# Kernel tuning notes

Measured on AMD Instinct MI355X. Metric: run time of the kernel, lower is better.

Reference implementation:

```python
import jax, jax.numpy as jnp
import numpy as np

N, E, G, H, L, GD = 100000, 1600000, 64, 128, 3, 32
NEG_SLOPE = 0.2
EPS = 1e-5


def setup_inputs() -> dict:
    key = jax.random.key(0)
    ks = jax.random.split(key, 10)
    s = 1.0 / np.sqrt(H)
    return {
        "x": jax.random.normal(ks[0], (N, H), jnp.float32),
        "global_feat": jax.random.normal(ks[1], (G, GD), jnp.float32),
        "W_src": jax.random.normal(ks[2], (L, H, H), jnp.float32) * s,
        "W_dst": jax.random.normal(ks[3], (L, H, H), jnp.float32) * s,
        "att": jax.random.normal(ks[4], (L, H), jnp.float32) * s,
        "b_conv": jnp.zeros((L, H), jnp.float32),
        "gn_w": jnp.ones((L, H), jnp.float32),
        "gn_b": jnp.zeros((L, H), jnp.float32),
        "gn_ms": jnp.ones((L, H), jnp.float32),
        "W1": jax.random.normal(ks[5], (H * L + GD, H), jnp.float32) * (1.0 / np.sqrt(H * L + GD)),
        "b1": jnp.zeros((H,), jnp.float32),
        "W2": jax.random.normal(ks[6], (H, 1), jnp.float32) * s,
        "b2": jnp.zeros((1,), jnp.float32),
        "edge_index": jax.random.randint(ks[7], (2, E), 0, N, jnp.int64),
        "batch": jnp.sort(jax.random.randint(ks[8], (N,), 0, G, jnp.int64)),
    }


def reference(x, global_feat, W_src, W_dst, att, b_conv, gn_w, gn_b, gn_ms,
              W1, b1, W2, b2, edge_index, batch):
    n = x.shape[0]
    g = global_feat.shape[0]
    layers = W_src.shape[0]
    loops = jnp.arange(n, dtype=edge_index.dtype)
    src = jnp.concatenate([edge_index[0], loops])  # add_self_loops=True
    dst = jnp.concatenate([edge_index[1], loops])
    counts = jnp.maximum(
        jax.ops.segment_sum(jnp.ones((n,), x.dtype), batch, num_segments=g), 1.0)

    outs = []
    for l in range(layers):
        # --- GATv2Conv (heads=1) ---
        xl = x @ W_src[l]          # source transform [N,H]
        xr = x @ W_dst[l]          # target transform [N,H]
        e = jax.nn.leaky_relu(xl[src] + xr[dst], NEG_SLOPE) @ att[l]  # [Etot]
        emax = jax.ops.segment_max(e, dst, num_segments=n)
        ex = jnp.exp(e - emax[dst])
        denom = jax.ops.segment_sum(ex, dst, num_segments=n)
        alpha = ex / denom[dst]
        h = jax.ops.segment_sum(alpha[:, None] * xl[src], dst, num_segments=n) + b_conv[l]
        # --- GraphNorm ---
        mean = jax.ops.segment_sum(h, batch, num_segments=g) / counts[:, None]
        sub = h - gn_ms[l] * mean[batch]
        var = jax.ops.segment_sum(sub * sub, batch, num_segments=g) / counts[:, None]
        h = gn_w[l] * sub * jax.lax.rsqrt(var[batch] + EPS) + gn_b[l]
        x = jax.nn.relu(h)
        # --- global_mean_pool ---
        outs.append(jax.ops.segment_sum(x, batch, num_segments=g) / counts[:, None])

    hcat = jnp.concatenate(outs + [global_feat], axis=1)  # JK cat + global feats
    z = jax.nn.relu(hcat @ W1 + b1)  # dropout = identity (eval)
    return z @ W2 + b2
```

## Files before the change

### kernel.cpp

```cpp
#include <hip/hip_runtime.h>
#include <hip/hip_bf16.h>
#include <math.h>

#define N_    100000
#define E_    1600000
#define ETOT_ 1700000
#define G_    64
#define H_    128
#define L_    3
#define GD_   32
#define NEG_  0.2f
#define EPS_  1e-5f

#define NBUK_ 391
#define CH_   8192
#define MCH_  196

typedef unsigned short ushort_t;
typedef unsigned int uint_t;
typedef __attribute__((ext_vector_type(4))) float f32x4;
typedef __attribute__((ext_vector_type(8))) short bf16x8;
typedef __attribute__((ext_vector_type(8))) unsigned short ushort8;

__device__ __forceinline__ ushort_t bfb(float f) {
    __hip_bfloat16 h = __float2bfloat16(f);
    return *reinterpret_cast<ushort_t*>(&h);
}


__global__ void k_init(float* pooled, int* gstart, const int* __restrict__ batch) {
    int i = blockIdx.x * 256 + threadIdx.x;
    if (i < L_ * G_ * H_) pooled[i] = 0.f;
    if (i <= G_) {
        int lo = 0, hi = N_;
        while (lo < hi) { int mid = (lo + hi) >> 1; if (batch[mid] < i) lo = mid + 1; else hi = mid; }
        gstart[i] = lo;
    }
}


__global__ __launch_bounds__(256) void k_bcount(const int* __restrict__ edst, int* __restrict__ C) {
    __shared__ int hist[NBUK_];
    int t = threadIdx.x, m = blockIdx.x;
    for (int i = t; i < NBUK_; i += 256) hist[i] = 0;
    __syncthreads();
    int base = m * CH_;
#pragma unroll
    for (int j = 0; j < CH_ / 256; j++) {
        int e = base + j * 256 + t;
        if (e < E_) atomicAdd(&hist[edst[e] >> 8], 1);
    }
    __syncthreads();
    for (int i = t; i < NBUK_; i += 256) C[i * MCH_ + m] = hist[i];
}

__global__ __launch_bounds__(256) void k_bscan(int* __restrict__ C, int* __restrict__ bucketEdges) {
    __shared__ int arr[256];
    int b = blockIdx.x, t = threadIdx.x;
    int v = (t < MCH_) ? C[b * MCH_ + t] : 0;
    arr[t] = v;
    __syncthreads();
    for (int off = 1; off < 256; off <<= 1) {
        int x = (t >= off) ? arr[t - off] : 0;
        __syncthreads();
        arr[t] += x;
        __syncthreads();
    }
    if (t < MCH_) C[b * MCH_ + t] = arr[t] - v;
    if (t == 255) bucketEdges[b] = arr[255];
}

__global__ __launch_bounds__(512) void k_bscan2(const int* __restrict__ bucketEdges,
                                                int* __restrict__ bstartE, int* __restrict__ bstartT,
                                                int* __restrict__ rowptr) {
    __shared__ int aE[512], aT[512];
    int t = threadIdx.x;
    int e = 0, tot = 0;
    if (t < NBUK_) {
        e = bucketEdges[t];
        int nib = N_ - t * 256; if (nib > 256) nib = 256;
        tot = e + nib;
    }
    aE[t] = e; aT[t] = tot;
    __syncthreads();
    for (int off = 1; off < 512; off <<= 1) {
        int xe = (t >= off) ? aE[t - off] : 0;
        int xt = (t >= off) ? aT[t - off] : 0;
        __syncthreads();
        aE[t] += xe; aT[t] += xt;
        __syncthreads();
    }
    if (t < NBUK_) { bstartE[t] = aE[t] - e; bstartT[t] = aT[t] - tot; }
    if (t == 0) rowptr[N_] = ETOT_;
}

__global__ __launch_bounds__(256) void k_bscatter(const int* __restrict__ esrc, const int* __restrict__ edst,
                                                  const int* __restrict__ C, const int* __restrict__ bstartE,
                                                  int2* __restrict__ stag) {
    __shared__ int cur[NBUK_];
    int t = threadIdx.x, m = blockIdx.x;
    for (int i = t; i < NBUK_; i += 256) cur[i] = C[i * MCH_ + m] + bstartE[i];
    __syncthreads();
    int base = m * CH_;
#pragma unroll
    for (int j = 0; j < CH_ / 256; j++) {
        int e = base + j * 256 + t;
        if (e < E_) {
            int s = esrc[e], d = edst[e];
            int pos = atomicAdd(&cur[d >> 8], 1);
            int2 p; p.x = s; p.y = d;
            stag[pos] = p;
        }
    }
}

__global__ __launch_bounds__(256) void k_bfinal(const int2* __restrict__ stag,
                                                const int* __restrict__ bucketEdges,
                                                const int* __restrict__ bstartE, const int* __restrict__ bstartT,
                                                int* __restrict__ rowptr, int* __restrict__ colarr) {
    __shared__ int deg[256];
    __shared__ int cursor[256];
    int b = blockIdx.x, t = threadIdx.x;
    int nb0 = b * 256;
    int nib = N_ - nb0; if (nib > 256) nib = 256;
    int ebeg = bstartE[b], ecnt = bucketEdges[b];
    deg[t] = (t < nib) ? 1 : 0;
    __syncthreads();
    for (int i = t; i < ecnt; i += 256) {
        int2 p = stag[ebeg + i];
        atomicAdd(&deg[p.y - nb0], 1);
    }
    __syncthreads();
    int v = deg[t];
    cursor[t] = v;
    __syncthreads();
    for (int off = 1; off < 256; off <<= 1) {
        int x = (t >= off) ? cursor[t - off] : 0;
        __syncthreads();
        cursor[t] += x;
        __syncthreads();
    }
    int excl = cursor[t] - v;
    int rowbase = bstartT[b];
    if (t < nib) {
        rowptr[nb0 + t] = rowbase + excl;
        colarr[rowbase + excl] = nb0 + t;
    }
    __syncthreads();
    cursor[t] = excl + 1;
    __syncthreads();
    for (int i = t; i < ecnt; i += 256) {
        int2 p = stag[ebeg + i];
        int pos = atomicAdd(&cursor[p.y - nb0], 1);
        colarr[rowbase + pos] = p.x;
    }
}


__global__ void k_cvt(const float* __restrict__ x, ushort_t* __restrict__ xb) {
    int i = blockIdx.x * 256 + threadIdx.x;
    float4 v = *(const float4*)(x + (size_t)i * 4);
    ushort4 o;
    o.x = bfb(v.x); o.y = bfb(v.y); o.z = bfb(v.z); o.w = bfb(v.w);
    *(ushort4*)(xb + (size_t)i * 4) = o;
}

__global__ void k_prep_w(const float* __restrict__ Ws, const float* __restrict__ Wd,
                         ushort_t* __restrict__ Wt) {
    int i = blockIdx.x * 256 + threadIdx.x;
    if (i >= L_ * 256 * H_) return;
    int l = i >> 15;
    int r = i & 32767;
    int c = r >> 7, k = r & 127;
    float v = (c < H_) ? Ws[(size_t)l * H_ * H_ + k * H_ + c]
                       : Wd[(size_t)l * H_ * H_ + k * H_ + (c - H_)];
    Wt[i] = bfb(v);
}


__global__ __launch_bounds__(256) void k_mfma(const ushort_t* __restrict__ xb,
                                              const ushort_t* __restrict__ Wt,
                                              ushort_t* __restrict__ xlb,
                                              float* __restrict__ xr) {
    int wv = threadIdx.x >> 6, lane = threadIdx.x & 63;
    int wt = blockIdx.x * 4 + wv;
    int row0 = wt * 16;
    if (row0 >= N_) return;
    int sl = lane & 15, q = lane >> 4;

    bf16x8 a[4];
    const ushort_t* ap = xb + (size_t)(row0 + sl) * H_ + q * 8;
#pragma unroll
    for (int kk = 0; kk < 4; kk++) a[kk] = *(const bf16x8*)(ap + kk * 32);

    f32x4 acc[16];
#pragma unroll
    for (int c = 0; c < 16; c++) acc[c] = (f32x4){0.f, 0.f, 0.f, 0.f};

#pragma unroll
    for (int c = 0; c < 16; c++) {
        const ushort_t* bp = Wt + (size_t)(c * 16 + sl) * H_ + q * 8;
#pragma unroll
        for (int kk = 0; kk < 4; kk++) {
            bf16x8 b = *(const bf16x8*)(bp + kk * 32);
            acc[c] = __builtin_amdgcn_mfma_f32_16x16x32_bf16(a[kk], b, acc[c], 0, 0, 0);
        }
    }

    int orow = row0 + q * 4;
#pragma unroll
    for (int c = 0; c < 8; c++)
#pragma unroll
        for (int j = 0; j < 4; j++)
            xlb[(size_t)(orow + j) * H_ + c * 16 + sl] = bfb(acc[c][j]);
#pragma unroll
    for (int c = 8; c < 16; c++)
#pragma unroll
        for (int j = 0; j < 4; j++)
            xr[(size_t)(orow + j) * H_ + (c - 8) * 16 + sl] = acc[c][j];
}


__global__ __launch_bounds__(256) void k_conv(const ushort_t* __restrict__ xlb, const float* __restrict__ xr,
                                              const int* __restrict__ rowptr, const int* __restrict__ colarr,
                                              const float* __restrict__ attl, const float* __restrict__ bcl,
                                              float* __restrict__ h) {
    int tid = threadIdx.x;
    int lane = tid & 63, wv = tid >> 6;
    int sl = lane & 15, q = lane >> 4;
    int row = blockIdx.x * 16 + wv * 4 + q;
    int d0 = sl * 8;

    float xrv[8], av[8], av5[8];
    {
        float4 t0 = *(const float4*)(xr + (size_t)row * H_ + d0);
        float4 t1 = *(const float4*)(xr + (size_t)row * H_ + d0 + 4);
        xrv[0] = t0.x; xrv[1] = t0.y; xrv[2] = t0.z; xrv[3] = t0.w;
        xrv[4] = t1.x; xrv[5] = t1.y; xrv[6] = t1.z; xrv[7] = t1.w;
        float4 a0 = *(const float4*)(attl + d0);
        float4 a1 = *(const float4*)(attl + d0 + 4);
        av[0] = a0.x; av[1] = a0.y; av[2] = a0.z; av[3] = a0.w;
        av[4] = a1.x; av[5] = a1.y; av[6] = a1.z; av[7] = a1.w;
#pragma unroll
        for (int e = 0; e < 8; e++) av5[e] = NEG_ * av[e];
    }

    int jb = rowptr[row];
    int n = rowptr[row + 1] - jb;

    float ssum = 0.f;
    float ac[8] = {0.f, 0.f, 0.f, 0.f, 0.f, 0.f, 0.f, 0.f};

    int s = (n > 0) ? colarr[jb] : 0;
    for (int i = 0; i < n; i++) {
        int snext = (i + 1 < n) ? colarr[jb + i + 1] : 0;
        ushort8 u = *(const ushort8*)(xlb + (size_t)s * H_ + d0);
        float v[8];
        float p = 0.f;
#pragma unroll
        for (int e = 0; e < 8; e++) {
            v[e] = __uint_as_float(((uint_t)u[e]) << 16);
            float t = v[e] + xrv[e];
            p = fmaf(t, (t > 0.f ? av[e] : av5[e]), p);
        }
        p += __shfl_xor(p, 8);
        p += __shfl_xor(p, 4);
        p += __shfl_xor(p, 2);
        p += __shfl_xor(p, 1);
        float wgt = __expf(p);
        ssum += wgt;
#pragma unroll
        for (int e = 0; e < 8; e++) ac[e] = fmaf(wgt, v[e], ac[e]);
        s = snext;
    }

    float inv = 1.f / ssum;
    float4 b0 = *(const float4*)(bcl + d0);
    float4 b1 = *(const float4*)(bcl + d0 + 4);
    float4 o0 = { ac[0] * inv + b0.x, ac[1] * inv + b0.y, ac[2] * inv + b0.z, ac[3] * inv + b0.w };
    float4 o1 = { ac[4] * inv + b1.x, ac[5] * inv + b1.y, ac[6] * inv + b1.z, ac[7] * inv + b1.w };
    *(float4*)(h + (size_t)row * H_ + d0) = o0;
    *(float4*)(h + (size_t)row * H_ + d0 + 4) = o1;
}


__global__ void k_zero_gn(float* gsum, float* gsq) {
    int i = blockIdx.x * 256 + threadIdx.x;
    if (i < G_ * H_) { gsum[i] = 0.f; gsq[i] = 0.f; }
}

__global__ void k_gn_stat(const float* __restrict__ h, const int* __restrict__ batch,
                          float* gsum, float* gsq) {
    int tid = threadIdx.x;
    int nb = blockIdx.x * 64;
    int d = tid & 127, hh = tid >> 7;
    int nend = nb + 64; if (nend > N_) nend = N_;
    float s1 = 0.f, s2 = 0.f; int curg = -1;
    for (int n = nb + hh; n < nend; n += 2) {
        int g = batch[n];
        if (g != curg) {
            if (curg >= 0) { atomicAdd(&gsum[curg * H_ + d], s1); atomicAdd(&gsq[curg * H_ + d], s2); }
            s1 = 0.f; s2 = 0.f; curg = g;
        }
        float v = h[(size_t)n * H_ + d];
        s1 += v; s2 += v * v;
    }
    if (curg >= 0) { atomicAdd(&gsum[curg * H_ + d], s1); atomicAdd(&gsq[curg * H_ + d], s2); }
}

__global__ void k_gn_fin(float* gsum, float* gsq, const int* __restrict__ gstart,
                         const float* __restrict__ gnwl, const float* __restrict__ gnmsl) {
    int i = blockIdx.x * 256 + threadIdx.x;
    if (i < G_ * H_) {
        int g = i >> 7, d = i & 127;
        int c = gstart[g + 1] - gstart[g]; if (c < 1) c = 1;
        float ic = 1.f / (float)c;
        float mean = gsum[i] * ic;
        float e2   = gsq[i] * ic;
        float ms = gnmsl[d];
        float var = e2 - ms * (2.f - ms) * mean * mean;
        gsum[i] = ms * mean;
        gsq[i]  = gnwl[d] * rsqrtf(var + EPS_);
    }
}

__global__ void k_gn_apply(const float* __restrict__ h, const int* __restrict__ batch,
                           const float* __restrict__ gmv, const float* __restrict__ giv,
                           const float* __restrict__ gnbl,
                           ushort_t* __restrict__ hb, float* pooled_l) {
    int tid = threadIdx.x;
    int nb = blockIdx.x * 64;
    int d = tid & 127, hh = tid >> 7;
    int nend = nb + 64; if (nend > N_) nend = N_;
    float bb = gnbl[d];
    float pacc = 0.f; int curg = -1; float mv = 0.f, iv = 0.f;
    for (int n = nb + hh; n < nend; n += 2) {
        int g = batch[n];
        if (g != curg) {
            if (curg >= 0) atomicAdd(&pooled_l[curg * H_ + d], pacc);
            pacc = 0.f; curg = g;
            mv = gmv[g * H_ + d];
            iv = giv[g * H_ + d];
        }
        float v = (h[(size_t)n * H_ + d] - mv) * iv + bb;
        v = fmaxf(v, 0.f);
        hb[(size_t)n * H_ + d] = bfb(v);
        pacc += v;
    }
    if (curg >= 0) atomicAdd(&pooled_l[curg * H_ + d], pacc);
}


__global__ __launch_bounds__(128) void k_mlp(const float* __restrict__ pooled, const float* __restrict__ gfeat,
                                             const int* __restrict__ gstart,
                                             const float* __restrict__ W1, const float* __restrict__ b1,
                                             const float* __restrict__ W2, const float* __restrict__ b2,
                                             float* __restrict__ out) {
    int g = blockIdx.x;
    int c = threadIdx.x;
    __shared__ float hc[H_ * L_ + GD_];
    __shared__ float zz[H_];
    int cn = gstart[g + 1] - gstart[g]; if (cn < 1) cn = 1;
    float ic = 1.f / (float)cn;
    for (int k = c; k < H_ * L_; k += 128)
        hc[k] = pooled[(k >> 7) * G_ * H_ + g * H_ + (k & 127)] * ic;
    if (c < GD_) hc[H_ * L_ + c] = gfeat[g * GD_ + c];
    __syncthreads();
    float z = b1[c];
#pragma unroll 4
    for (int k = 0; k < H_ * L_ + GD_; k++)
        z += hc[k] * W1[k * H_ + c];
    z = fmaxf(z, 0.f);
    zz[c] = z * W2[c];
    __syncthreads();
    for (int off = 64; off > 0; off >>= 1) {
        if (c < off) zz[c] += zz[c + off];
        __syncthreads();
    }
    if (c == 0) out[g] = zz[0] + b2[0];
}


extern "C" void kernel_launch(void* const* d_in, const int* in_sizes, int n_in,
                              void* d_out, int out_size, void* d_ws, size_t ws_size,
                              hipStream_t stream) {
    const float* x0    = (const float*)d_in[0];
    const float* gfeat = (const float*)d_in[1];
    const float* Wsrc  = (const float*)d_in[2];
    const float* Wdst  = (const float*)d_in[3];
    const float* att   = (const float*)d_in[4];
    const float* bconv = (const float*)d_in[5];
    const float* gnw   = (const float*)d_in[6];
    const float* gnb   = (const float*)d_in[7];
    const float* gnms  = (const float*)d_in[8];
    const float* W1    = (const float*)d_in[9];
    const float* b1    = (const float*)d_in[10];
    const float* W2    = (const float*)d_in[11];
    const float* b2    = (const float*)d_in[12];
    const int*   eidx  = (const int*)d_in[13];
    const int*   batch = (const int*)d_in[14];
    const int* esrc = eidx;
    const int* edst = eidx + E_;
    float* out = (float*)d_out;

    char* w = (char*)d_ws;
    size_t off = 0;
    auto alloc = [&](size_t bytes) { char* p = w + off; off += (bytes + 255) & ~(size_t)255; return p; };
    ushort_t* xb    = (ushort_t*)alloc((size_t)N_ * H_ * 2);
    ushort_t* xlb   = (ushort_t*)alloc((size_t)N_ * H_ * 2);
    float* xr     = (float*)alloc((size_t)N_ * H_ * 4);
    float* hbuf   = (float*)alloc((size_t)N_ * H_ * 4);
    ushort_t* Wt    = (ushort_t*)alloc((size_t)L_ * 256 * H_ * 2);
    int*   rowptr = (int*)alloc((size_t)(N_ + 1) * 4);
    int*   colarr = (int*)alloc((size_t)ETOT_ * 4);
    int*   bktE   = (int*)alloc(NBUK_ * 4);
    int*   bstartE= (int*)alloc(NBUK_ * 4);
    int*   bstartT= (int*)alloc(NBUK_ * 4);
    int*   gstart = (int*)alloc((G_ + 1) * 4);
    float* gsum   = (float*)alloc(G_ * H_ * 4);
    float* gsq    = (float*)alloc(G_ * H_ * 4);
    float* pooled = (float*)alloc((size_t)L_ * G_ * H_ * 4);
    int2* stag = (int2*)xr;
    int*  C    = (int*)hbuf;
    (void)ws_size; (void)in_sizes; (void)n_in; (void)out_size;

    k_init<<<(N_ + 255) / 256, 256, 0, stream>>>(pooled, gstart, batch);
    k_bcount<<<MCH_, 256, 0, stream>>>(edst, C);
    k_bscan<<<NBUK_, 256, 0, stream>>>(C, bktE);
    k_bscan2<<<1, 512, 0, stream>>>(bktE, bstartE, bstartT, rowptr);
    k_bscatter<<<MCH_, 256, 0, stream>>>(esrc, edst, C, bstartE, stag);
    k_bfinal<<<NBUK_, 256, 0, stream>>>(stag, bktE, bstartE, bstartT, rowptr, colarr);

    k_cvt<<<(N_ * H_ / 4 + 255) / 256, 256, 0, stream>>>(x0, xb);
    k_prep_w<<<(L_ * 256 * H_ + 255) / 256, 256, 0, stream>>>(Wsrc, Wdst, Wt);

    for (int l = 0; l < L_; l++) {
        k_mfma<<<(N_ / 16 + 3) / 4, 256, 0, stream>>>(xb, Wt + (size_t)l * 256 * H_, xlb, xr);
        k_conv<<<N_ / 16, 256, 0, stream>>>(xlb, xr, rowptr, colarr,
                                            att + (size_t)l * H_, bconv + (size_t)l * H_, hbuf);
        k_zero_gn<<<(G_ * H_ + 255) / 256, 256, 0, stream>>>(gsum, gsq);
        k_gn_stat<<<(N_ + 63) / 64, 256, 0, stream>>>(hbuf, batch, gsum, gsq);
        k_gn_fin<<<(G_ * H_ + 255) / 256, 256, 0, stream>>>(gsum, gsq, gstart,
                                                            gnw + (size_t)l * H_, gnms + (size_t)l * H_);
        k_gn_apply<<<(N_ + 63) / 64, 256, 0, stream>>>(hbuf, batch, gsum, gsq,
                                                       gnb + (size_t)l * H_, xb,
                                                       pooled + (size_t)l * G_ * H_);
    }

    k_mlp<<<G_, 128, 0, stream>>>(pooled, gfeat, gstart, W1, b1, W2, b2, out);
}
```

Baseline: 645.1 us.

## Fuse GraphNorm stats into conv, apply norm in next GEMM, store bf16 intermediates

Folds the GraphNorm statistic accumulation into the attention conv epilogue, using block-level shared reductions when all 16 rows share a graph. The normalize+ReLU step moves into the next layer's MFMA input load, so the pooling kernel only reads h and no longer writes xb. The x-to-bf16 conversion is folded into the first GEMM. xr and h are now stored as bf16 instead of fp32, which lowers memory traffic at some precision cost. The edge-bucketing chunk size is also shrunk to give more blocks. The aim is fewer kernel launches and fewer full passes over N×H arrays, at the cost of statistics computed from fp32 values while h is stored rounded to bf16.

```diff
diff --git a/kernel.cpp b/kernel.cpp
--- a/kernel.cpp
+++ b/kernel.cpp
@@ -7,14 +7,15 @@
 #define ETOT_ 1700000
 #define G_    64
 #define H_    128
+#define GH_   8192
 #define L_    3
 #define GD_   32
 #define NEG_  0.2f
 #define EPS_  1e-5f
 
 #define NBUK_ 391
-#define CH_   8192
-#define MCH_  196
+#define CH_   2048
+#define MCH_  782
 
 typedef unsigned short ushort_t;
 typedef unsigned int uint_t;
@@ -26,11 +27,15 @@
     __hip_bfloat16 h = __float2bfloat16(f);
     return *reinterpret_cast<ushort_t*>(&h);
 }
-
-
-__global__ void k_init(float* pooled, int* gstart, const int* __restrict__ batch) {
+__device__ __forceinline__ float uf(ushort_t u) {
+    return __uint_as_float(((uint_t)u) << 16);
+}
+
+
+__global__ void k_init(float* pooled, float* gsum, float* gsq, int* gstart,
+                       const int* __restrict__ batch) {
     int i = blockIdx.x * 256 + threadIdx.x;
-    if (i < L_ * G_ * H_) pooled[i] = 0.f;
+    if (i < L_ * GH_) { pooled[i] = 0.f; gsum[i] = 0.f; gsq[i] = 0.f; }
     if (i <= G_) {
         int lo = 0, hi = N_;
         while (lo < hi) { int mid = (lo + hi) >> 1; if (batch[mid] < i) lo = mid + 1; else hi = mid; }
@@ -54,20 +59,20 @@
     for (int i = t; i < NBUK_; i += 256) C[i * MCH_ + m] = hist[i];
 }
 
-__global__ __launch_bounds__(256) void k_bscan(int* __restrict__ C, int* __restrict__ bucketEdges) {
-    __shared__ int arr[256];
+__global__ __launch_bounds__(1024) void k_bscan(int* __restrict__ C, int* __restrict__ bucketEdges) {
+    __shared__ int arr[1024];
     int b = blockIdx.x, t = threadIdx.x;
     int v = (t < MCH_) ? C[b * MCH_ + t] : 0;
     arr[t] = v;
     __syncthreads();
-    for (int off = 1; off < 256; off <<= 1) {
+    for (int off = 1; off < 1024; off <<= 1) {
         int x = (t >= off) ? arr[t - off] : 0;
         __syncthreads();
         arr[t] += x;
         __syncthreads();
     }
     if (t < MCH_) C[b * MCH_ + t] = arr[t] - v;
-    if (t == 255) bucketEdges[b] = arr[255];
+    if (t == 1023) bucketEdges[b] = arr[1023];
 }
 
 __global__ __launch_bounds__(512) void k_bscan2(const int* __restrict__ bucketEdges,
@@ -157,14 +162,6 @@
 }
 
 
-__global__ void k_cvt(const float* __restrict__ x, ushort_t* __restrict__ xb) {
-    int i = blockIdx.x * 256 + threadIdx.x;
-    float4 v = *(const float4*)(x + (size_t)i * 4);
-    ushort4 o;
-    o.x = bfb(v.x); o.y = bfb(v.y); o.z = bfb(v.z); o.w = bfb(v.w);
-    *(ushort4*)(xb + (size_t)i * 4) = o;
-}
-
 __global__ void k_prep_w(const float* __restrict__ Ws, const float* __restrict__ Wd,
                          ushort_t* __restrict__ Wt) {
     int i = blockIdx.x * 256 + threadIdx.x;
@@ -178,20 +175,63 @@
 }
 
 
-__global__ __launch_bounds__(256) void k_mfma(const ushort_t* __restrict__ xb,
-                                              const ushort_t* __restrict__ Wt,
-                                              ushort_t* __restrict__ xlb,
-                                              float* __restrict__ xr) {
+template<int FIRST>
+__global__ __launch_bounds__(256) void k_mfma_t(const float* __restrict__ x0,
+                                                const ushort_t* __restrict__ hin,
+                                                const int* __restrict__ batch,
+                                                const float* __restrict__ mv,
+                                                const float* __restrict__ iv,
+                                                const float* __restrict__ bb,
+                                                const ushort_t* __restrict__ Wt,
+                                                ushort_t* __restrict__ xlb,
+                                                ushort_t* __restrict__ xrb) {
     int wv = threadIdx.x >> 6, lane = threadIdx.x & 63;
-    int wt = blockIdx.x * 4 + wv;
-    int row0 = wt * 16;
+    int row0 = (blockIdx.x * 4 + wv) * 16;
     if (row0 >= N_) return;
     int sl = lane & 15, q = lane >> 4;
+    int row = row0 + sl;
 
     bf16x8 a[4];
-    const ushort_t* ap = xb + (size_t)(row0 + sl) * H_ + q * 8;
-#pragma unroll
-    for (int kk = 0; kk < 4; kk++) a[kk] = *(const bf16x8*)(ap + kk * 32);
+    if (FIRST) {
+        const float* ap = x0 + (size_t)row * H_ + q * 8;
+#pragma unroll
+        for (int kk = 0; kk < 4; kk++) {
+            float4 v0 = *(const float4*)(ap + kk * 32);
+            float4 v1 = *(const float4*)(ap + kk * 32 + 4);
+            bf16x8 t;
+            t[0] = (short)bfb(v0.x); t[1] = (short)bfb(v0.y);
+            t[2] = (short)bfb(v0.z); t[3] = (short)bfb(v0.w);
+            t[4] = (short)bfb(v1.x); t[5] = (short)bfb(v1.y);
+            t[6] = (short)bfb(v1.z); t[7] = (short)bfb(v1.w);
+            a[kk] = t;
+        }
+    } else {
+        int g = batch[row];
+        const ushort_t* hp = hin + (size_t)row * H_ + q * 8;
+        const float* mvp = mv + g * H_ + q * 8;
+        const float* ivp = iv + g * H_ + q * 8;
+        const float* bbp = bb + q * 8;
+#pragma unroll
+        for (int kk = 0; kk < 4; kk++) {
+            ushort8 u = *(const ushort8*)(hp + kk * 32);
+            float4 m0 = *(const float4*)(mvp + kk * 32);
+            float4 m1 = *(const float4*)(mvp + kk * 32 + 4);
+            float4 i0 = *(const float4*)(ivp + kk * 32);
+            float4 i1 = *(const float4*)(ivp + kk * 32 + 4);
+            float4 c0 = *(const float4*)(bbp + kk * 32);
+            float4 c1 = *(const float4*)(bbp + kk * 32 + 4);
+            bf16x8 t;
+            t[0] = (short)bfb(fmaxf((uf(u[0]) - m0.x) * i0.x + c0.x, 0.f));
+            t[1] = (short)bfb(fmaxf((uf(u[1]) - m0.y) * i0.y + c0.y, 0.f));
+            t[2] = (short)bfb(fmaxf((uf(u[2]) - m0.z) * i0.z + c0.z, 0.f));
+            t[3] = (short)bfb(fmaxf((uf(u[3]) - m0.w) * i0.w + c0.w, 0.f));
+            t[4] = (short)bfb(fmaxf((uf(u[4]) - m1.x) * i1.x + c1.x, 0.f));
+            t[5] = (short)bfb(fmaxf((uf(u[5]) - m1.y) * i1.y + c1.y, 0.f));
+            t[6] = (short)bfb(fmaxf((uf(u[6]) - m1.z) * i1.z + c1.z, 0.f));
+            t[7] = (short)bfb(fmaxf((uf(u[7]) - m1.w) * i1.w + c1.w, 0.f));
+            a[kk] = t;
+        }
+    }
 
     f32x4 acc[16];
 #pragma unroll
@@ -217,15 +257,22 @@
     for (int c = 8; c < 16; c++)
 #pragma unroll
         for (int j = 0; j < 4; j++)
-            xr[(size_t)(orow + j) * H_ + (c - 8) * 16 + sl] = acc[c][j];
-}
-
-
-__global__ __launch_bounds__(256) void k_conv(const ushort_t* __restrict__ xlb, const float* __restrict__ xr,
+            xrb[(size_t)(orow + j) * H_ + (c - 8) * 16 + sl] = bfb(acc[c][j]);
+}
+
+
+__global__ __launch_bounds__(256) void k_conv(const ushort_t* __restrict__ xlb,
+                                              const ushort_t* __restrict__ xrb,
                                               const int* __restrict__ rowptr, const int* __restrict__ colarr,
                                               const float* __restrict__ attl, const float* __restrict__ bcl,
-                                              float* __restrict__ h) {
+                                              const int* __restrict__ batch,
+                                              ushort_t* __restrict__ h,
+                                              float* __restrict__ gsum, float* __restrict__ gsq) {
+    __shared__ float ls1[H_], ls2[H_];
     int tid = threadIdx.x;
+    if (tid < H_) { ls1[tid] = 0.f; ls2[tid] = 0.f; }
+    __syncthreads();
+
     int lane = tid & 63, wv = tid >> 6;
     int sl = lane & 15, q = lane >> 4;
     int row = blockIdx.x * 16 + wv * 4 + q;
@@ -233,16 +280,13 @@
 
     float xrv[8], av[8], av5[8];
     {
-        float4 t0 = *(const float4*)(xr + (size_t)row * H_ + d0);
-        float4 t1 = *(const float4*)(xr + (size_t)row * H_ + d0 + 4);
-        xrv[0] = t0.x; xrv[1] = t0.y; xrv[2] = t0.z; xrv[3] = t0.w;
-        xrv[4] = t1.x; xrv[5] = t1.y; xrv[6] = t1.z; xrv[7] = t1.w;
+        ushort8 ux = *(const ushort8*)(xrb + (size_t)row * H_ + d0);
         float4 a0 = *(const float4*)(attl + d0);
         float4 a1 = *(const float4*)(attl + d0 + 4);
         av[0] = a0.x; av[1] = a0.y; av[2] = a0.z; av[3] = a0.w;
         av[4] = a1.x; av[5] = a1.y; av[6] = a1.z; av[7] = a1.w;
 #pragma unroll
-        for (int e = 0; e < 8; e++) av5[e] = NEG_ * av[e];
+        for (int e = 0; e < 8; e++) { xrv[e] = uf(ux[e]); av5[e] = NEG_ * av[e]; }
     }
 
     int jb = rowptr[row];
@@ -259,7 +303,7 @@
         float p = 0.f;
 #pragma unroll
         for (int e = 0; e < 8; e++) {
-            v[e] = __uint_as_float(((uint_t)u[e]) << 16);
+            v[e] = uf(u[e]);
             float t = v[e] + xrv[e];
             p = fmaf(t, (t > 0.f ? av[e] : av5[e]), p);
         }
@@ -277,41 +321,54 @@
     float inv = 1.f / ssum;
     float4 b0 = *(const float4*)(bcl + d0);
     float4 b1 = *(const float4*)(bcl + d0 + 4);
-    float4 o0 = { ac[0] * inv + b0.x, ac[1] * inv + b0.y, ac[2] * inv + b0.z, ac[3] * inv + b0.w };
-    float4 o1 = { ac[4] * inv + b1.x, ac[5] * inv + b1.y, ac[6] * inv + b1.z, ac[7] * inv + b1.w };
-    *(float4*)(h + (size_t)row * H_ + d0) = o0;
-    *(float4*)(h + (size_t)row * H_ + d0 + 4) = o1;
-}
-
-
-__global__ void k_zero_gn(float* gsum, float* gsq) {
-    int i = blockIdx.x * 256 + threadIdx.x;
-    if (i < G_ * H_) { gsum[i] = 0.f; gsq[i] = 0.f; }
-}
-
-__global__ void k_gn_stat(const float* __restrict__ h, const int* __restrict__ batch,
-                          float* gsum, float* gsq) {
-    int tid = threadIdx.x;
-    int nb = blockIdx.x * 64;
-    int d = tid & 127, hh = tid >> 7;
-    int nend = nb + 64; if (nend > N_) nend = N_;
-    float s1 = 0.f, s2 = 0.f; int curg = -1;
-    for (int n = nb + hh; n < nend; n += 2) {
-        int g = batch[n];
-        if (g != curg) {
-            if (curg >= 0) { atomicAdd(&gsum[curg * H_ + d], s1); atomicAdd(&gsq[curg * H_ + d], s2); }
-            s1 = 0.f; s2 = 0.f; curg = g;
-        }
-        float v = h[(size_t)n * H_ + d];
-        s1 += v; s2 += v * v;
-    }
-    if (curg >= 0) { atomicAdd(&gsum[curg * H_ + d], s1); atomicAdd(&gsq[curg * H_ + d], s2); }
-}
+    float o[8];
+    o[0] = ac[0] * inv + b0.x; o[1] = ac[1] * inv + b0.y;
+    o[2] = ac[2] * inv + b0.z; o[3] = ac[3] * inv + b0.w;
+    o[4] = ac[4] * inv + b1.x; o[5] = ac[5] * inv + b1.y;
+    o[6] = ac[6] * inv + b1.z; o[7] = ac[7] * inv + b1.w;
+
+    ushort8 ho;
+#pragma unroll
+    for (int e = 0; e < 8; e++) ho[e] = bfb(o[e]);
+    *(ushort8*)(h + (size_t)row * H_ + d0) = ho;
+
+    float s1[8], s2[8];
+#pragma unroll
+    for (int e = 0; e < 8; e++) { s1[e] = o[e]; s2[e] = o[e] * o[e]; }
+
+    int g0 = batch[blockIdx.x * 16];
+    int g1 = batch[blockIdx.x * 16 + 15];
+    if (g0 == g1) {
+#pragma unroll
+        for (int e = 0; e < 8; e++) {
+            s1[e] += __shfl_xor(s1[e], 16); s1[e] += __shfl_xor(s1[e], 32);
+            s2[e] += __shfl_xor(s2[e], 16); s2[e] += __shfl_xor(s2[e], 32);
+        }
+        if (q == 0) {
+#pragma unroll
+            for (int e = 0; e < 8; e++) {
+                atomicAdd(&ls1[d0 + e], s1[e]);
+                atomicAdd(&ls2[d0 + e], s2[e]);
+            }
+        }
+        __syncthreads();
+        if (tid < H_) atomicAdd(&gsum[g0 * H_ + tid], ls1[tid]);
+        else if (tid < 2 * H_) atomicAdd(&gsq[g0 * H_ + tid - H_], ls2[tid - H_]);
+    } else {
+        int g = batch[row];
+#pragma unroll
+        for (int e = 0; e < 8; e++) {
+            atomicAdd(&gsum[g * H_ + d0 + e], s1[e]);
+            atomicAdd(&gsq[g * H_ + d0 + e], s2[e]);
+        }
+    }
+}
+
 
 __global__ void k_gn_fin(float* gsum, float* gsq, const int* __restrict__ gstart,
                          const float* __restrict__ gnwl, const float* __restrict__ gnmsl) {
     int i = blockIdx.x * 256 + threadIdx.x;
-    if (i < G_ * H_) {
+    if (i < GH_) {
         int g = i >> 7, d = i & 127;
         int c = gstart[g + 1] - gstart[g]; if (c < 1) c = 1;
         float ic = 1.f / (float)c;
@@ -324,30 +381,39 @@
     }
 }
 
-__global__ void k_gn_apply(const float* __restrict__ h, const int* __restrict__ batch,
-                           const float* __restrict__ gmv, const float* __restrict__ giv,
-                           const float* __restrict__ gnbl,
-                           ushort_t* __restrict__ hb, float* pooled_l) {
+
+__global__ void k_pool(const ushort_t* __restrict__ h, const int* __restrict__ batch,
+                       const float* __restrict__ mv, const float* __restrict__ iv,
+                       const float* __restrict__ bb, float* __restrict__ pooled_l) {
     int tid = threadIdx.x;
     int nb = blockIdx.x * 64;
-    int d = tid & 127, hh = tid >> 7;
+    int d2 = (tid & 63) * 2, hh = tid >> 6;
     int nend = nb + 64; if (nend > N_) nend = N_;
-    float bb = gnbl[d];
-    float pacc = 0.f; int curg = -1; float mv = 0.f, iv = 0.f;
-    for (int n = nb + hh; n < nend; n += 2) {
+    float b0 = bb[d2], b1 = bb[d2 + 1];
+    float p0 = 0.f, p1 = 0.f; int curg = -1;
+    float m0 = 0.f, m1 = 0.f, i0 = 0.f, i1 = 0.f;
+    for (int n = nb + hh; n < nend; n += 4) {
         int g = batch[n];
         if (g != curg) {
-            if (curg >= 0) atomicAdd(&pooled_l[curg * H_ + d], pacc);
-            pacc = 0.f; curg = g;
-            mv = gmv[g * H_ + d];
-            iv = giv[g * H_ + d];
-        }
-        float v = (h[(size_t)n * H_ + d] - mv) * iv + bb;
-        v = fmaxf(v, 0.f);
-        hb[(size_t)n * H_ + d] = bfb(v);
-        pacc += v;
-    }
-    if (curg >= 0) atomicAdd(&pooled_l[curg * H_ + d], pacc);
+            if (curg >= 0) {
+                atomicAdd(&pooled_l[curg * H_ + d2], p0);
+                atomicAdd(&pooled_l[curg * H_ + d2 + 1], p1);
+            }
+            p0 = 0.f; p1 = 0.f; curg = g;
+            m0 = mv[g * H_ + d2]; m1 = mv[g * H_ + d2 + 1];
+            i0 = iv[g * H_ + d2]; i1 = iv[g * H_ + d2 + 1];
+        }
+        uint_t u = *(const uint_t*)(h + (size_t)n * H_ + d2);
+        float v0 = __uint_as_float(u << 16);
+        float v1 = __uint_as_float(u & 0xffff0000u);
+        v0 = fmaxf((v0 - m0) * i0 + b0, 0.f);
+        v1 = fmaxf((v1 - m1) * i1 + b1, 0.f);
+        p0 += v0; p1 += v1;
+    }
+    if (curg >= 0) {
+        atomicAdd(&pooled_l[curg * H_ + d2], p0);
+        atomicAdd(&pooled_l[curg * H_ + d2 + 1], p1);
+    }
 }
 
 
@@ -363,7 +429,7 @@
     int cn = gstart[g + 1] - gstart[g]; if (cn < 1) cn = 1;
     float ic = 1.f / (float)cn;
     for (int k = c; k < H_ * L_; k += 128)
-        hc[k] = pooled[(k >> 7) * G_ * H_ + g * H_ + (k & 127)] * ic;
+        hc[k] = pooled[(k >> 7) * GH_ + g * H_ + (k & 127)] * ic;
     if (c < GD_) hc[H_ * L_ + c] = gfeat[g * GD_ + c];
     __syncthreads();
     float z = b1[c];
@@ -406,45 +472,51 @@
     char* w = (char*)d_ws;
     size_t off = 0;
     auto alloc = [&](size_t bytes) { char* p = w + off; off += (bytes + 255) & ~(size_t)255; return p; };
-    ushort_t* xb    = (ushort_t*)alloc((size_t)N_ * H_ * 2);
-    ushort_t* xlb   = (ushort_t*)alloc((size_t)N_ * H_ * 2);
-    float* xr     = (float*)alloc((size_t)N_ * H_ * 4);
-    float* hbuf   = (float*)alloc((size_t)N_ * H_ * 4);
-    ushort_t* Wt    = (ushort_t*)alloc((size_t)L_ * 256 * H_ * 2);
-    int*   rowptr = (int*)alloc((size_t)(N_ + 1) * 4);
-    int*   colarr = (int*)alloc((size_t)ETOT_ * 4);
-    int*   bktE   = (int*)alloc(NBUK_ * 4);
-    int*   bstartE= (int*)alloc(NBUK_ * 4);
-    int*   bstartT= (int*)alloc(NBUK_ * 4);
-    int*   gstart = (int*)alloc((G_ + 1) * 4);
-    float* gsum   = (float*)alloc(G_ * H_ * 4);
-    float* gsq    = (float*)alloc(G_ * H_ * 4);
-    float* pooled = (float*)alloc((size_t)L_ * G_ * H_ * 4);
-    int2* stag = (int2*)xr;
-    int*  C    = (int*)hbuf;
+    ushort_t* xlb  = (ushort_t*)alloc((size_t)N_ * H_ * 2);
+    ushort_t* xrb  = (ushort_t*)alloc((size_t)N_ * H_ * 2);
+    ushort_t* h    = (ushort_t*)alloc((size_t)N_ * H_ * 2);
+    ushort_t* Wt   = (ushort_t*)alloc((size_t)L_ * 256 * H_ * 2);
+    int*   rowptr  = (int*)alloc((size_t)(N_ + 1) * 4);
+    int*   colarr  = (int*)alloc((size_t)ETOT_ * 4);
+    int*   bktE    = (int*)alloc(NBUK_ * 4);
+    int*   bstartE = (int*)alloc(NBUK_ * 4);
+    int*   bstartT = (int*)alloc(NBUK_ * 4);
+    int*   gstart  = (int*)alloc((G_ + 1) * 4);
+    float* gsum    = (float*)alloc((size_t)L_ * GH_ * 4);
+    float* gsq     = (float*)alloc((size_t)L_ * GH_ * 4);
+    float* pooled  = (float*)alloc((size_t)L_ * GH_ * 4);
+    int2* stag = (int2*)xlb;
+    int*  C    = (int*)xrb;
     (void)ws_size; (void)in_sizes; (void)n_in; (void)out_size;
 
-    k_init<<<(N_ + 255) / 256, 256, 0, stream>>>(pooled, gstart, batch);
+    k_init<<<(N_ + 255) / 256, 256, 0, stream>>>(pooled, gsum, gsq, gstart, batch);
     k_bcount<<<MCH_, 256, 0, stream>>>(edst, C);
-    k_bscan<<<NBUK_, 256, 0, stream>>>(C, bktE);
+    k_bscan<<<NBUK_, 1024, 0, stream>>>(C, bktE);
     k_bscan2<<<1, 512, 0, stream>>>(bktE, bstartE, bstartT, rowptr);
     k_bscatter<<<MCH_, 256, 0, stream>>>(esrc, edst, C, bstartE, stag);
     k_bfinal<<<NBUK_, 256, 0, stream>>>(stag, bktE, bstartE, bstartT, rowptr, colarr);
-
-    k_cvt<<<(N_ * H_ / 4 + 255) / 256, 256, 0, stream>>>(x0, xb);
     k_prep_w<<<(L_ * 256 * H_ + 255) / 256, 256, 0, stream>>>(Wsrc, Wdst, Wt);
 
+    int mfma_grid = (N_ / 16 + 3) / 4;
     for (int l = 0; l < L_; l++) {
-        k_mfma<<<(N_ / 16 + 3) / 4, 256, 0, stream>>>(xb, Wt + (size_t)l * 256 * H_, xlb, xr);
-        k_conv<<<N_ / 16, 256, 0, stream>>>(xlb, xr, rowptr, colarr,
-                                            att + (size_t)l * H_, bconv + (size_t)l * H_, hbuf);
-        k_zero_gn<<<(G_ * H_ + 255) / 256, 256, 0, stream>>>(gsum, gsq);
-        k_gn_stat<<<(N_ + 63) / 64, 256, 0, stream>>>(hbuf, batch, gsum, gsq);
-        k_gn_fin<<<(G_ * H_ + 255) / 256, 256, 0, stream>>>(gsum, gsq, gstart,
-                                                            gnw + (size_t)l * H_, gnms + (size_t)l * H_);
-        k_gn_apply<<<(N_ + 63) / 64, 256, 0, stream>>>(hbuf, batch, gsum, gsq,
-                                                       gnb + (size_t)l * H_, xb,
-                                                       pooled + (size_t)l * G_ * H_);
+        if (l == 0)
+            k_mfma_t<1><<<mfma_grid, 256, 0, stream>>>(x0, h, batch, gsum, gsq, gnb,
+                                                       Wt, xlb, xrb);
+        else
+            k_mfma_t<0><<<mfma_grid, 256, 0, stream>>>(x0, h, batch,
+                                                       gsum + (size_t)(l - 1) * GH_,
+                                                       gsq + (size_t)(l - 1) * GH_,
+                                                       gnb + (size_t)(l - 1) * H_,
+                                                       Wt + (size_t)l * 256 * H_, xlb, xrb);
+        k_conv<<<N_ / 16, 256, 0, stream>>>(xlb, xrb, rowptr, colarr,
+                                            att + (size_t)l * H_, bconv + (size_t)l * H_,
+                                            batch, h,
+                                            gsum + (size_t)l * GH_, gsq + (size_t)l * GH_);
+        k_gn_fin<<<GH_ / 256, 256, 0, stream>>>(gsum + (size_t)l * GH_, gsq + (size_t)l * GH_,
+                                                gstart, gnw + (size_t)l * H_, gnms + (size_t)l * H_);
+        k_pool<<<(N_ + 63) / 64, 256, 0, stream>>>(h, batch,
+                                                   gsum + (size_t)l * GH_, gsq + (size_t)l * GH_,
+                                                   gnb + (size_t)l * H_, pooled + (size_t)l * GH_);
     }
 
     k_mlp<<<G_, 128, 0, stream>>>(pooled, gfeat, gstart, W1, b1, W2, b2, out);
```

Measured after the change: 741.1 us. 1.15x slower.
